# Kernel optimization log

Measured on AMD Instinct MI355X. Metric: run time of the kernel, lower is better.

## Reference

```python
import jax, jax.numpy as jnp
import numpy as np

B, IN_CH, N, DIM, PH, HID, K = 4, 128, 2048, 256, 64, 1024, 16
EPS = 1e-5


def conv1(x, w, b):
    # 1x1 Conv1d: x (B,C,N), w (O,C) -> (B,O,N)
    return jnp.einsum('oc,bcn->bon', w, x) + b[None, :, None]


def conv2(x, w, b):
    # 1x1 Conv2d: x (B,C,N,K), w (O,C) -> (B,O,N,K)
    return jnp.einsum('oc,bcnk->bonk', w, x) + b[None, :, None, None]


def bn2(x, g, beta, mean, var):
    # eval-mode BatchNorm2d over channel dim of (B,C,N,K)
    scale = g * jax.lax.rsqrt(var + EPS)
    return x * scale[None, :, None, None] + (beta - mean * scale)[None, :, None, None]


def query_knn(pos, k):
    # pos: (B,3,N). Returns (B,N,K) indices of k nearest neighbors (incl. self).
    p = jnp.transpose(pos, (0, 2, 1))                     # (B,N,3)
    sq = jnp.sum(p * p, axis=-1)                          # (B,N)
    dist = sq[:, :, None] + sq[:, None, :] - 2.0 * jnp.einsum('bnc,bmc->bnm', p, p)
    _, idx = jax.lax.top_k(-dist, k)                      # smallest distances first
    return idx


def group(feat, idx):
    # feat: (B,C,N), idx: (B,N,K) -> (B,C,N,K) where out[b,c,i,k]=feat[b,c,idx[b,i,k]]
    b, c, n = feat.shape
    k = idx.shape[-1]
    ib = jnp.broadcast_to(idx.reshape(b, 1, n * k), (b, c, n * k))
    return jnp.take_along_axis(feat, ib, axis=2).reshape(b, c, n, k)


def setup_inputs() -> dict:
    key = jax.random.key(0)
    ks = jax.random.split(key, 12)
    s = 0.02
    return {
        'x': jax.random.normal(ks[0], (B, IN_CH, N), jnp.float32),
        'pos': jax.random.normal(ks[1], (B, 3, N), jnp.float32),
        'ls_w': jax.random.normal(ks[2], (DIM, IN_CH), jnp.float32) * s,
        'ls_b': jnp.zeros((DIM,), jnp.float32),
        'kw': jax.random.normal(ks[3], (DIM, DIM), jnp.float32) * s,
        'kb': jnp.zeros((DIM,), jnp.float32),
        'qw': jax.random.normal(ks[4], (DIM, DIM), jnp.float32) * s,
        'qb': jnp.zeros((DIM,), jnp.float32),
        'vw': jax.random.normal(ks[5], (DIM, DIM), jnp.float32) * s,
        'vb': jnp.zeros((DIM,), jnp.float32),
        'pw1': jax.random.normal(ks[6], (PH, 3), jnp.float32) * s,
        'pb1': jnp.zeros((PH,), jnp.float32),
        'pg': jnp.ones((PH,), jnp.float32),
        'pbeta': jnp.zeros((PH,), jnp.float32),
        'pmean': jnp.zeros((PH,), jnp.float32),
        'pvar': jnp.ones((PH,), jnp.float32),
        'pw2': jax.random.normal(ks[7], (DIM, PH), jnp.float32) * s,
        'pb2': jnp.zeros((DIM,), jnp.float32),
        'aw1': jax.random.normal(ks[8], (HID, DIM), jnp.float32) * s,
        'ab1': jnp.zeros((HID,), jnp.float32),
        'ag': jnp.ones((HID,), jnp.float32),
        'abeta': jnp.zeros((HID,), jnp.float32),
        'amean': jnp.zeros((HID,), jnp.float32),
        'avar': jnp.ones((HID,), jnp.float32),
        'aw2': jax.random.normal(ks[9], (DIM, HID), jnp.float32) * s,
        'ab2': jnp.zeros((DIM,), jnp.float32),
        'lw': jax.random.normal(ks[10], (IN_CH, DIM), jnp.float32) * s,
        'lb': jnp.zeros((IN_CH,), jnp.float32),
    }


def reference(x, pos, ls_w, ls_b, kw, kb, qw, qb, vw, vb,
              pw1, pb1, pg, pbeta, pmean, pvar, pw2, pb2,
              aw1, ab1, ag, abeta, amean, avar, aw2, ab2, lw, lb):
    identity = x
    h = conv1(x, ls_w, ls_b)                              # (B,DIM,N)
    idx = query_knn(pos, K)                               # (B,N,K) int32
    key_f = group(conv1(h, kw, kb), idx)                  # (B,DIM,N,K)
    value = conv1(h, vw, vb)                              # (B,DIM,N)
    query = conv1(h, qw, qb)                              # (B,DIM,N)
    qk_rel = query[:, :, :, None] - key_f                 # (B,DIM,N,K)
    pos_rel = pos[:, :, :, None] - group(pos, idx)        # (B,3,N,K)
    pe = conv2(jax.nn.relu(bn2(conv2(pos_rel, pw1, pb1), pg, pbeta, pmean, pvar)), pw2, pb2)
    attn = conv2(jax.nn.relu(bn2(conv2(qk_rel + pe, aw1, ab1), ag, abeta, amean, avar)), aw2, ab2)
    attn = jax.nn.softmax(attn, axis=-1)                  # softmax over K
    val_g = group(value, idx) + pe                        # (B,DIM,N,K)
    agg = jnp.sum(attn * val_g, axis=-1)                  # (B,DIM,N)
    y = conv1(agg, lw, lb)                                # (B,IN_CH,N)
    return y + identity
```

## Files before the change

kernel.cpp:

```cpp
#include <hip/hip_runtime.h>
#include <hip/hip_bf16.h>
#include <math.h>

#define B_    4
#define CIN   128
#define NPTS  2048
#define DIM   256
#define PH    64
#define HIDN  1024
#define KNN_  16
#define BN    (B_*NPTS)
#define CC    (BN*KNN_)
#define EPS_  1e-5f

typedef __bf16 bf16;
typedef __bf16 bf16x8 __attribute__((ext_vector_type(8)));
typedef __bf16 bf16x4 __attribute__((ext_vector_type(4)));
typedef float  f32x4  __attribute__((ext_vector_type(4)));

__global__ __launch_bounds__(256) void prep_kernel(
    const float* __restrict__ ls_w, const float* __restrict__ kw,
    const float* __restrict__ qw,   const float* __restrict__ vw,
    const float* __restrict__ pw2,  const float* __restrict__ aw1,
    const float* __restrict__ aw2,  const float* __restrict__ lw,
    const float* __restrict__ pb1,  const float* __restrict__ pg,
    const float* __restrict__ pbeta,const float* __restrict__ pmean,
    const float* __restrict__ pvar,
    const float* __restrict__ ab1,  const float* __restrict__ ag,
    const float* __restrict__ abeta,const float* __restrict__ amean,
    const float* __restrict__ avar,
    bf16* ls_wb, bf16* kwb, bf16* qwb, bf16* vwb,
    bf16* pw2b, bf16* aw1b, bf16* aw2b, bf16* lwb,
    float* pe_scale, float* pe_shift, float* at_scale, float* at_shift)
{
  long e = (long)blockIdx.x * 256 + threadIdx.x;
  if (e < 32768)  { ls_wb[e] = (bf16)ls_w[e]; return; } e -= 32768;
  if (e < 65536)  { kwb[e]   = (bf16)kw[e];   return; } e -= 65536;
  if (e < 65536)  { qwb[e]   = (bf16)qw[e];   return; } e -= 65536;
  if (e < 65536)  { vwb[e]   = (bf16)vw[e];   return; } e -= 65536;
  if (e < 16384)  { pw2b[e]  = (bf16)pw2[e];  return; } e -= 16384;
  if (e < 262144) { aw1b[e]  = (bf16)aw1[e];  return; } e -= 262144;
  if (e < 262144) { aw2b[e]  = (bf16)aw2[e];  return; } e -= 262144;
  if (e < 32768)  { lwb[e]   = (bf16)lw[e];   return; } e -= 32768;
  if (e < 64) {
    float sc = pg[e] * rsqrtf(pvar[e] + EPS_);
    pe_scale[e] = sc;
    pe_shift[e] = sc * pb1[e] + pbeta[e] - pmean[e] * sc;
    return;
  } e -= 64;
  if (e < 1024) {
    float sc = ag[e] * rsqrtf(avar[e] + EPS_);
    at_scale[e] = sc;
    at_shift[e] = sc * ab1[e] + abeta[e] - amean[e] * sc;
  }
}

__global__ __launch_bounds__(256) void transpose_x_kernel(
    const float* __restrict__ x, bf16* __restrict__ xT)
{
  long e = (long)blockIdx.x * 256 + threadIdx.x;
  int ch = (int)(e & (CIN - 1));
  long i = e >> 7;
  int n = (int)(i & (NPTS - 1));
  int b = (int)(i >> 11);
  xT[e] = (bf16)x[((long)b * CIN + ch) * NPTS + n];
}

__global__ __launch_bounds__(256) void knn_kernel(
    const float* __restrict__ pos, int* __restrict__ idx_out)
{
  __shared__ float px[NPTS], py[NPTS], pz[NPTS];
  const int tid = threadIdx.x;
  const int lane = tid & 63, wave = tid >> 6;
  const int q = blockIdx.x * 4 + wave;
  const int b = q >> 11;
  const int n = q & (NPTS - 1);
  const float* p = pos + (long)b * 3 * NPTS;
  for (int j = tid; j < NPTS; j += 256) {
    px[j] = p[j]; py[j] = p[NPTS + j]; pz[j] = p[2 * NPTS + j];
  }
  __syncthreads();
  float qx = px[n], qy = py[n], qz = pz[n];
  float qs = qx * qx + qy * qy + qz * qz;
  float d[32];
#pragma unroll
  for (int j = 0; j < 32; ++j) {
    int pt = j * 64 + lane;
    float x = px[pt], y = py[pt], z = pz[pt];
    float s2 = x * x + y * y + z * z;
    float dt = qx * x + qy * y + qz * z;
    d[j] = qs + s2 - 2.f * dt;
  }
  for (int r = 0; r < KNN_; ++r) {
    float bv = 1e30f; int bj = 0;
#pragma unroll
    for (int j = 0; j < 32; ++j)
      if (d[j] < bv) { bv = d[j]; bj = j; }
    int bi = bj * 64 + lane;
#pragma unroll
    for (int off = 32; off >= 1; off >>= 1) {
      float ov = __shfl_xor(bv, off);
      int   oi = __shfl_xor(bi, off);
      if (ov < bv || (ov == bv && oi < bi)) { bv = ov; bi = oi; }
    }
    if (lane == 0) idx_out[(long)q * KNN_ + r] = bi;
#pragma unroll
    for (int j = 0; j < 32; ++j)
      if (bi == j * 64 + lane) d[j] = 1e30f;
  }
}

template<int KD, bool OBF16>
__global__ __launch_bounds__(256) void gemmT_kernel(
    const bf16* __restrict__ inT, const bf16* __restrict__ Wb,
    const float* __restrict__ bias, void* __restrict__ outp, int O)
{
  const int tid = threadIdx.x;
  const int lane = tid & 63, wave = tid >> 6;
  const int row16 = lane & 15, grp = lane >> 4;
  const long i0 = (long)blockIdx.x * 64 + (wave & 1) * 32;
  const long o0 = (long)blockIdx.y * 64 + (wave >> 1) * 32;
  f32x4 acc[2][2] = {};
  const bf16* a0p = inT + (i0 + row16) * KD + grp * 8;
  const bf16* a1p = a0p + 16 * KD;
  const bf16* b0p = Wb + (o0 + row16) * KD + grp * 8;
  const bf16* b1p = b0p + 16 * KD;
#pragma unroll
  for (int ks = 0; ks < KD / 32; ++ks) {
    bf16x8 a0 = *(const bf16x8*)(a0p + ks * 32);
    bf16x8 a1 = *(const bf16x8*)(a1p + ks * 32);
    bf16x8 b0 = *(const bf16x8*)(b0p + ks * 32);
    bf16x8 b1 = *(const bf16x8*)(b1p + ks * 32);
    acc[0][0] = __builtin_amdgcn_mfma_f32_16x16x32_bf16(a0, b0, acc[0][0], 0, 0, 0);
    acc[0][1] = __builtin_amdgcn_mfma_f32_16x16x32_bf16(a0, b1, acc[0][1], 0, 0, 0);
    acc[1][0] = __builtin_amdgcn_mfma_f32_16x16x32_bf16(a1, b0, acc[1][0], 0, 0, 0);
    acc[1][1] = __builtin_amdgcn_mfma_f32_16x16x32_bf16(a1, b1, acc[1][1], 0, 0, 0);
  }
#pragma unroll
  for (int ot = 0; ot < 2; ++ot) {
    long o = o0 + ot * 16 + row16;
    float bv = bias[o];
#pragma unroll
    for (int it = 0; it < 2; ++it) {
#pragma unroll
      for (int r = 0; r < 4; ++r) {
        long i = i0 + it * 16 + grp * 4 + r;
        float v = acc[it][ot][r] + bv;
        if (OBF16) ((bf16*)outp)[i * O + o] = (bf16)v;
        else       ((float*)outp)[i * O + o] = v;
      }
    }
  }
}

__global__ __launch_bounds__(512, 4) void attn_fused_kernel(
    const bf16* __restrict__ qT, const bf16* __restrict__ kT,
    const bf16* __restrict__ vTb, const float* __restrict__ pos,
    const int* __restrict__ idx, const float* __restrict__ pw1,
    const float* __restrict__ pe_scale, const float* __restrict__ pe_shift,
    const bf16* __restrict__ pw2b, const float* __restrict__ pb2,
    const bf16* __restrict__ aw1b, const bf16* __restrict__ aw2b,
    const float* __restrict__ at_scale, const float* __restrict__ at_shift,
    const float* __restrict__ ab2, bf16* __restrict__ aggT)
{
  __shared__ __align__(16) bf16 u_lds[64 * 256];
  __shared__ __align__(16) bf16 tbuf[64 * 128];
  __shared__ float rel_lds[64][4];
  __shared__ int   idx_lds[64];
  bf16* t_lds   = tbuf;
  bf16* hid_lds = tbuf;

  const int tid = threadIdx.x;
  const int lane = tid & 63, wave = tid >> 6;
  const int row16 = lane & 15, grp = lane >> 4;
  const int r7 = row16 & 7;
  const long c0 = (long)blockIdx.x * 64;
  const int bn0 = blockIdx.x * 4;
  const int b = bn0 >> 11;
  const float* pB = pos + (long)b * 3 * NPTS;
  const int os = wave * 32;

  if (tid < 64) {
    int nb = idx[c0 + tid];
    idx_lds[tid] = nb;
    int n = (bn0 + (tid >> 4)) & (NPTS - 1);
    rel_lds[tid][0] = pB[n] - pB[nb];
    rel_lds[tid][1] = pB[NPTS + n] - pB[NPTS + nb];
    rel_lds[tid][2] = pB[2 * NPTS + n] - pB[2 * NPTS + nb];
  }
#pragma unroll
  for (int it = 0; it < 4; ++it) {
    int id = it * 512 + tid;
    int col = id >> 5, ch16 = id & 31;
    int nb = idx[c0 + col];
    *(bf16x8*)&u_lds[col * 256 + ((ch16 ^ (col & 7)) << 3)] =
        *(const bf16x8*)(kT + ((long)b * NPTS + nb) * DIM + ch16 * 8);
  }
  __syncthreads();

  {
    int c = tid & 63, jq = tid >> 6;
    float rx = rel_lds[c][0], ry = rel_lds[c][1], rz = rel_lds[c][2];
    bf16x8 pk8;
#pragma unroll
    for (int jj = 0; jj < 8; ++jj) {
      int j = jq * 8 + jj;
      float v = pw1[j * 3] * rx + pw1[j * 3 + 1] * ry + pw1[j * 3 + 2] * rz;
      v = pe_scale[j] * v + pe_shift[j];
      pk8[jj] = (bf16)fmaxf(v, 0.f);
    }
    *(bf16x8*)&hid_lds[c * 64 + ((jq ^ (c & 7)) << 3)] = pk8;
  }
  __syncthreads();

  f32x4 accpe[4][2] = {};
#pragma unroll
  for (int ks = 0; ks < 2; ++ks) {
    bf16x8 ah[4];
#pragma unroll
    for (int ct = 0; ct < 4; ++ct)
      ah[ct] = *(const bf16x8*)&hid_lds[(ct * 16 + row16) * 64 + (((ks * 4 + grp) ^ r7) << 3)];
#pragma unroll
    for (int ot = 0; ot < 2; ++ot) {
      bf16x8 bw = *(const bf16x8*)(pw2b + (long)(os + ot * 16 + row16) * PH + ks * 32 + grp * 8);
#pragma unroll
      for (int ct = 0; ct < 4; ++ct)
        accpe[ct][ot] = __builtin_amdgcn_mfma_f32_16x16x32_bf16(ah[ct], bw, accpe[ct][ot], 0, 0, 0);
    }
  }

  bf16x4 pe_bf[4][2];
#pragma unroll
  for (int ot = 0; ot < 2; ++ot) {
    int o = os + ot * 16 + row16;
    float pb2v = pb2[o];
#pragma unroll
    for (int ct = 0; ct < 4; ++ct) {
      float qv = (float)qT[(long)(bn0 + ct) * DIM + o];
#pragma unroll
      for (int r = 0; r < 4; ++r) {
        int c = ct * 16 + grp * 4 + r;
        int ua = c * 256 + (((o >> 3) ^ (c & 7)) << 3) + (o & 7);
        float pev = accpe[ct][ot][r] + pb2v;
        float kv = (float)u_lds[ua];
        u_lds[ua] = (bf16)(qv - kv + pev);
        pe_bf[ct][ot][r] = (bf16)pev;
      }
    }
  }
  __syncthreads();

  const int hs16 = wave * 16;
  f32x4 acc2[4][2] = {};
  for (int jp = 0; jp < 4; ++jp) {
    const int hg0 = (2 * jp) * 128 + hs16;
    const int hg1 = hg0 + 128;
    f32x4 acc1a[4] = {}, acc1b[4] = {};
    const bf16* awp0 = aw1b + (long)(hg0 + row16) * DIM + grp * 8;
    const bf16* awp1 = awp0 + 128 * DIM;
#pragma unroll 2
    for (int ks = 0; ks < 8; ++ks) {
      bf16x8 awA = *(const bf16x8*)(awp0 + ks * 32);
      bf16x8 awB = *(const bf16x8*)(awp1 + ks * 32);
      const int ublk = ((ks * 4 + grp) ^ r7) << 3;
#pragma unroll
      for (int ct = 0; ct < 4; ++ct) {
        bf16x8 bu = *(const bf16x8*)&u_lds[(ct * 16 + row16) * 256 + ublk];
        acc1a[ct] = __builtin_amdgcn_mfma_f32_16x16x32_bf16(awA, bu, acc1a[ct], 0, 0, 0);
        acc1b[ct] = __builtin_amdgcn_mfma_f32_16x16x32_bf16(awB, bu, acc1b[ct], 0, 0, 0);
      }
    }
#pragma unroll
    for (int half = 0; half < 2; ++half) {
      const int hg = half ? hg1 : hg0;
      const int jcbase = (2 * jp + half) * 128;
      f32x4 sc4 = *(const f32x4*)&at_scale[hg + grp * 4];
      f32x4 sh4 = *(const f32x4*)&at_shift[hg + grp * 4];
#pragma unroll
      for (int ct = 0; ct < 4; ++ct) {
        const f32x4 a1 = half ? acc1b[ct] : acc1a[ct];
        bf16x4 pk;
#pragma unroll
        for (int r = 0; r < 4; ++r) {
          float v = sc4[r] * a1[r] + sh4[r];
          pk[r] = (bf16)fmaxf(v, 0.f);
        }
        int trow = ct * 16 + row16;
        int tblk = (wave * 2 + (grp >> 1)) ^ (trow & 7);
        *(bf16x4*)&t_lds[trow * 128 + (tblk << 3) + ((grp & 1) << 2)] = pk;
      }
      __syncthreads();
#pragma unroll
      for (int ks2 = 0; ks2 < 4; ++ks2) {
        bf16x8 b2;
#pragma unroll
        for (int ot = 0; ot < 2; ++ot) {
          b2 = *(const bf16x8*)(aw2b + (long)(os + ot * 16 + row16) * HIDN + jcbase + ks2 * 32 + grp * 8);
#pragma unroll
          for (int ct = 0; ct < 4; ++ct) {
            bf16x8 a2 = *(const bf16x8*)&t_lds[(ct * 16 + row16) * 128 + (((ks2 * 4 + grp) ^ r7) << 3)];
            acc2[ct][ot] = __builtin_amdgcn_mfma_f32_16x16x32_bf16(a2, b2, acc2[ct][ot], 0, 0, 0);
          }
        }
      }
      __syncthreads();
    }
  }

#pragma unroll
  for (int ct = 0; ct < 4; ++ct) {
#pragma unroll
    for (int ot = 0; ot < 2; ++ot) {
      int o = os + ot * 16 + row16;
      float ab = ab2[o];
      float l[4];
      float m = -1e30f;
#pragma unroll
      for (int r = 0; r < 4; ++r) {
        l[r] = acc2[ct][ot][r] + ab;
        m = fmaxf(m, l[r]);
      }
      m = fmaxf(m, __shfl_xor(m, 16));
      m = fmaxf(m, __shfl_xor(m, 32));
      float s = 0.f;
#pragma unroll
      for (int r = 0; r < 4; ++r) { l[r] = __expf(l[r] - m); s += l[r]; }
      s += __shfl_xor(s, 16);
      s += __shfl_xor(s, 32);
      float inv = 1.f / s;
      float agg = 0.f;
#pragma unroll
      for (int r = 0; r < 4; ++r) {
        int c = ct * 16 + grp * 4 + r;
        int nb = idx_lds[c];
        float vv = (float)vTb[((long)b * NPTS + nb) * DIM + o];
        agg += l[r] * (vv + (float)pe_bf[ct][ot][r]);
      }
      agg *= inv;
      agg += __shfl_xor(agg, 16);
      agg += __shfl_xor(agg, 32);
      if (grp == 0) aggT[(long)(bn0 + ct) * DIM + o] = (bf16)agg;
    }
  }
}

__global__ __launch_bounds__(256) void final_kernel(
    const bf16* __restrict__ aggT, const bf16* __restrict__ lwb,
    const float* __restrict__ lb, const float* __restrict__ x,
    float* __restrict__ out)
{
  const int tid = threadIdx.x;
  const int lane = tid & 63, wave = tid >> 6;
  const int row16 = lane & 15, grp = lane >> 4;
  const long i0 = (long)blockIdx.x * 64 + (wave & 1) * 32;
  const int o0 = blockIdx.y * 64 + (wave >> 1) * 32;
  f32x4 acc[2][2] = {};
  const bf16* a0p = aggT + (i0 + row16) * DIM + grp * 8;
  const bf16* a1p = a0p + 16 * DIM;
  const bf16* b0p = lwb + (long)(o0 + row16) * DIM + grp * 8;
  const bf16* b1p = b0p + 16 * DIM;
#pragma unroll
  for (int ks = 0; ks < 8; ++ks) {
    bf16x8 a0 = *(const bf16x8*)(a0p + ks * 32);
    bf16x8 a1 = *(const bf16x8*)(a1p + ks * 32);
    bf16x8 b0 = *(const bf16x8*)(b0p + ks * 32);
    bf16x8 b1 = *(const bf16x8*)(b1p + ks * 32);
    acc[0][0] = __builtin_amdgcn_mfma_f32_16x16x32_bf16(a0, b0, acc[0][0], 0, 0, 0);
    acc[0][1] = __builtin_amdgcn_mfma_f32_16x16x32_bf16(a0, b1, acc[0][1], 0, 0, 0);
    acc[1][0] = __builtin_amdgcn_mfma_f32_16x16x32_bf16(a1, b0, acc[1][0], 0, 0, 0);
    acc[1][1] = __builtin_amdgcn_mfma_f32_16x16x32_bf16(a1, b1, acc[1][1], 0, 0, 0);
  }
#pragma unroll
  for (int ot = 0; ot < 2; ++ot) {
    int o = o0 + ot * 16 + row16;
    float bv = lb[o];
#pragma unroll
    for (int it = 0; it < 2; ++it) {
#pragma unroll
      for (int r = 0; r < 4; ++r) {
        long i = i0 + it * 16 + grp * 4 + r;
        int bb = (int)(i >> 11);
        int n = (int)(i & (NPTS - 1));
        long off = ((long)bb * CIN + o) * NPTS + n;
        out[off] = acc[it][ot][r] + bv + x[off];
      }
    }
  }
}

extern "C" void kernel_launch(void* const* d_in, const int* in_sizes, int n_in,
                              void* d_out, int out_size, void* d_ws, size_t ws_size,
                              hipStream_t stream)
{
  const float* x     = (const float*)d_in[0];
  const float* pos   = (const float*)d_in[1];
  const float* ls_w  = (const float*)d_in[2];
  const float* ls_b  = (const float*)d_in[3];
  const float* kw    = (const float*)d_in[4];
  const float* kb    = (const float*)d_in[5];
  const float* qw    = (const float*)d_in[6];
  const float* qb    = (const float*)d_in[7];
  const float* vw    = (const float*)d_in[8];
  const float* vb    = (const float*)d_in[9];
  const float* pw1   = (const float*)d_in[10];
  const float* pb1   = (const float*)d_in[11];
  const float* pg    = (const float*)d_in[12];
  const float* pbeta = (const float*)d_in[13];
  const float* pmean = (const float*)d_in[14];
  const float* pvar  = (const float*)d_in[15];
  const float* pw2   = (const float*)d_in[16];
  const float* pb2   = (const float*)d_in[17];
  const float* aw1   = (const float*)d_in[18];
  const float* ab1   = (const float*)d_in[19];
  const float* ag    = (const float*)d_in[20];
  const float* abeta = (const float*)d_in[21];
  const float* amean = (const float*)d_in[22];
  const float* avar  = (const float*)d_in[23];
  const float* aw2   = (const float*)d_in[24];
  const float* ab2   = (const float*)d_in[25];
  const float* lw    = (const float*)d_in[26];
  const float* lb    = (const float*)d_in[27];

  char* ws = (char*)d_ws;
  size_t off = 0;
  auto alloc = [&](size_t bytes) -> void* {
    void* p = ws + off;
    off = (off + bytes + 255) & ~(size_t)255;
    return p;
  };

  bf16* ls_wb = (bf16*)alloc(32768 * 2);
  bf16* kwb   = (bf16*)alloc(65536 * 2);
  bf16* qwb   = (bf16*)alloc(65536 * 2);
  bf16* vwb   = (bf16*)alloc(65536 * 2);
  bf16* pw2b  = (bf16*)alloc(16384 * 2);
  bf16* aw1b  = (bf16*)alloc(262144 * 2);
  bf16* aw2b  = (bf16*)alloc(262144 * 2);
  bf16* lwb   = (bf16*)alloc(32768 * 2);
  float* pe_scale = (float*)alloc(64 * 4);
  float* pe_shift = (float*)alloc(64 * 4);
  float* at_scale = (float*)alloc(1024 * 4);
  float* at_shift = (float*)alloc(1024 * 4);
  int*  idx  = (int*)alloc((size_t)CC * 4);
  bf16* xT   = (bf16*)alloc((size_t)BN * CIN * 2);
  bf16* hT   = (bf16*)alloc((size_t)BN * DIM * 2);
  bf16* qT   = (bf16*)alloc((size_t)BN * DIM * 2);
  bf16* kT   = (bf16*)alloc((size_t)BN * DIM * 2);
  bf16* vTb  = (bf16*)alloc((size_t)BN * DIM * 2);
  bf16* aggT = (bf16*)alloc((size_t)BN * DIM * 2);

  prep_kernel<<<dim3((803904 + 255) / 256), 256, 0, stream>>>(
      ls_w, kw, qw, vw, pw2, aw1, aw2, lw,
      pb1, pg, pbeta, pmean, pvar, ab1, ag, abeta, amean, avar,
      ls_wb, kwb, qwb, vwb, pw2b, aw1b, aw2b, lwb,
      pe_scale, pe_shift, at_scale, at_shift);

  transpose_x_kernel<<<dim3(BN * CIN / 256), 256, 0, stream>>>(x, xT);

  knn_kernel<<<dim3(BN / 4), 256, 0, stream>>>(pos, idx);

  gemmT_kernel<128, true><<<dim3(BN / 64, DIM / 64), 256, 0, stream>>>(xT, ls_wb, ls_b, hT, DIM);

  gemmT_kernel<256, true><<<dim3(BN / 64, DIM / 64), 256, 0, stream>>>(hT, qwb, qb, qT, DIM);
  gemmT_kernel<256, true><<<dim3(BN / 64, DIM / 64), 256, 0, stream>>>(hT, kwb, kb, kT, DIM);
  gemmT_kernel<256, true><<<dim3(BN / 64, DIM / 64), 256, 0, stream>>>(hT, vwb, vb, vTb, DIM);

  attn_fused_kernel<<<dim3(CC / 64), 512, 0, stream>>>(
      qT, kT, vTb, pos, idx, pw1, pe_scale, pe_shift, pw2b, pb2,
      aw1b, aw2b, at_scale, at_shift, ab2, aggT);

  final_kernel<<<dim3(BN / 64, CIN / 64), 256, 0, stream>>>(aggT, lwb, lb, x, (float*)d_out);
}
```

Measured before the change: 495.4 us.

## Double-buffer hidden tile to overlap first and second attention GEMMs

Splits the hidden-dimension loop into 128-wide chunks and double-buffers the ReLU hidden tile in LDS. The next chunk's first GEMM is computed while the current chunk's second GEMM reads the other buffer, leaving one barrier per chunk instead of two. This doubles the tbuf LDS footprint (extra 16KB), which can lower occupancy under launch_bounds(512,4). It also drops the two-accumulator interleave in the first GEMM.

```diff
diff --git a/kernel.cpp b/kernel.cpp
--- a/kernel.cpp
+++ b/kernel.cpp
@@ -164,11 +164,10 @@
     const float* __restrict__ ab2, bf16* __restrict__ aggT)
 {
   __shared__ __align__(16) bf16 u_lds[64 * 256];
-  __shared__ __align__(16) bf16 tbuf[64 * 128];
+  __shared__ __align__(16) bf16 tbuf[2][64 * 128];
   __shared__ float rel_lds[64][4];
   __shared__ int   idx_lds[64];
-  bf16* t_lds   = tbuf;
-  bf16* hid_lds = tbuf;
+  bf16* hid_lds = tbuf[0];
 
   const int tid = threadIdx.x;
   const int lane = tid & 63, wave = tid >> 6;
@@ -252,59 +251,56 @@
 
   const int hs16 = wave * 16;
   f32x4 acc2[4][2] = {};
-  for (int jp = 0; jp < 4; ++jp) {
-    const int hg0 = (2 * jp) * 128 + hs16;
-    const int hg1 = hg0 + 128;
-    f32x4 acc1a[4] = {}, acc1b[4] = {};
-    const bf16* awp0 = aw1b + (long)(hg0 + row16) * DIM + grp * 8;
-    const bf16* awp1 = awp0 + 128 * DIM;
-#pragma unroll 2
+
+  auto do_gemm1 = [&](int jc) {
+    const int hg = jc * 128 + hs16;
+    const int buf = jc & 1;
+    f32x4 acc1[4] = {};
+    const bf16* awp = aw1b + (long)(hg + row16) * DIM + grp * 8;
+#pragma unroll
     for (int ks = 0; ks < 8; ++ks) {
-      bf16x8 awA = *(const bf16x8*)(awp0 + ks * 32);
-      bf16x8 awB = *(const bf16x8*)(awp1 + ks * 32);
+      bf16x8 aw = *(const bf16x8*)(awp + ks * 32);
       const int ublk = ((ks * 4 + grp) ^ r7) << 3;
 #pragma unroll
       for (int ct = 0; ct < 4; ++ct) {
         bf16x8 bu = *(const bf16x8*)&u_lds[(ct * 16 + row16) * 256 + ublk];
-        acc1a[ct] = __builtin_amdgcn_mfma_f32_16x16x32_bf16(awA, bu, acc1a[ct], 0, 0, 0);
-        acc1b[ct] = __builtin_amdgcn_mfma_f32_16x16x32_bf16(awB, bu, acc1b[ct], 0, 0, 0);
-      }
-    }
-#pragma unroll
-    for (int half = 0; half < 2; ++half) {
-      const int hg = half ? hg1 : hg0;
-      const int jcbase = (2 * jp + half) * 128;
-      f32x4 sc4 = *(const f32x4*)&at_scale[hg + grp * 4];
-      f32x4 sh4 = *(const f32x4*)&at_shift[hg + grp * 4];
-#pragma unroll
-      for (int ct = 0; ct < 4; ++ct) {
-        const f32x4 a1 = half ? acc1b[ct] : acc1a[ct];
-        bf16x4 pk;
-#pragma unroll
-        for (int r = 0; r < 4; ++r) {
-          float v = sc4[r] * a1[r] + sh4[r];
-          pk[r] = (bf16)fmaxf(v, 0.f);
+        acc1[ct] = __builtin_amdgcn_mfma_f32_16x16x32_bf16(aw, bu, acc1[ct], 0, 0, 0);
+      }
+    }
+    f32x4 sc4 = *(const f32x4*)&at_scale[hg + grp * 4];
+    f32x4 sh4 = *(const f32x4*)&at_shift[hg + grp * 4];
+#pragma unroll
+    for (int ct = 0; ct < 4; ++ct) {
+      bf16x4 pk;
+#pragma unroll
+      for (int r = 0; r < 4; ++r) {
+        float v = sc4[r] * acc1[ct][r] + sh4[r];
+        pk[r] = (bf16)fmaxf(v, 0.f);
+      }
+      int trow = ct * 16 + row16;
+      int tblk = (wave * 2 + (grp >> 1)) ^ (trow & 7);
+      *(bf16x4*)&tbuf[buf][trow * 128 + (tblk << 3) + ((grp & 1) << 2)] = pk;
+    }
+  };
+
+  do_gemm1(0);
+  __syncthreads();
+  for (int jc = 0; jc < 8; ++jc) {
+    if (jc < 7) do_gemm1(jc + 1);
+    const bf16* tb = tbuf[jc & 1];
+#pragma unroll
+    for (int ks2 = 0; ks2 < 4; ++ks2) {
+#pragma unroll
+      for (int ot = 0; ot < 2; ++ot) {
+        bf16x8 b2 = *(const bf16x8*)(aw2b + (long)(os + ot * 16 + row16) * HIDN + jc * 128 + ks2 * 32 + grp * 8);
+#pragma unroll
+        for (int ct = 0; ct < 4; ++ct) {
+          bf16x8 a2 = *(const bf16x8*)&tb[(ct * 16 + row16) * 128 + (((ks2 * 4 + grp) ^ r7) << 3)];
+          acc2[ct][ot] = __builtin_amdgcn_mfma_f32_16x16x32_bf16(a2, b2, acc2[ct][ot], 0, 0, 0);
         }
-        int trow = ct * 16 + row16;
-        int tblk = (wave * 2 + (grp >> 1)) ^ (trow & 7);
-        *(bf16x4*)&t_lds[trow * 128 + (tblk << 3) + ((grp & 1) << 2)] = pk;
-      }
-      __syncthreads();
-#pragma unroll
-      for (int ks2 = 0; ks2 < 4; ++ks2) {
-        bf16x8 b2;
-#pragma unroll
-        for (int ot = 0; ot < 2; ++ot) {
-          b2 = *(const bf16x8*)(aw2b + (long)(os + ot * 16 + row16) * HIDN + jcbase + ks2 * 32 + grp * 8);
-#pragma unroll
-          for (int ct = 0; ct < 4; ++ct) {
-            bf16x8 a2 = *(const bf16x8*)&t_lds[(ct * 16 + row16) * 128 + (((ks2 * 4 + grp) ^ r7) << 3)];
-            acc2[ct][ot] = __builtin_amdgcn_mfma_f32_16x16x32_bf16(a2, b2, acc2[ct][ot], 0, 0, 0);
-          }
-        }
-      }
-      __syncthreads();
-    }
+      }
+    }
+    __syncthreads();
   }
 
 #pragma unroll
```

New measurement: 491.1 us. Within noise of the previous version (-0.9%).
